# Optimization experiments

Measured on AMD Instinct MI355X. Metric: run time of the kernel, lower is better.

## Reference

```python
import jax, jax.numpy as jnp
import numpy as np

PC_RANGE = np.array([-15.0, -30.0, -2.0, 15.0, 30.0, 2.0], np.float32)
POST_CENTER = np.array([-20.0, -35.0, -20.0, -35.0, 20.0, 35.0, 20.0, 35.0], np.float32)
MAX_NUM = 100
NUM_CLASSES = 10
SCORE_THR = 0.1

_SX = PC_RANGE[3] - PC_RANGE[0]
_SY = PC_RANGE[4] - PC_RANGE[1]


def _denorm_bbox(b):
    # cxcywh -> xyxy, then scale x coords by pc_range x-extent, y by y-extent
    cx, cy, w, h = b[..., 0], b[..., 1], b[..., 2], b[..., 3]
    xyxy = jnp.stack([cx - w / 2, cy - h / 2, cx + w / 2, cy + h / 2], axis=-1)
    scale = jnp.asarray([_SX, _SY, _SX, _SY], jnp.float32)
    off = jnp.asarray([PC_RANGE[0], PC_RANGE[1], PC_RANGE[0], PC_RANGE[1]], jnp.float32)
    return xyxy * scale + off


def _denorm_pts(p):
    scale = jnp.asarray([_SX, _SY], jnp.float32)
    off = jnp.asarray([PC_RANGE[0], PC_RANGE[1]], jnp.float32)
    return p * scale + off


def _thresh_mask(scores):
    # torch: while thresh_mask.sum()==0: tmp*=0.9; if tmp<0.01: all-true; break
    s = jax.lax.stop_gradient(scores)
    mask0 = s > SCORE_THR

    def cond(state):
        _, m = state
        return jnp.sum(m) == 0

    def body(state):
        tmp, _ = state
        tmp = tmp * 0.9
        m = jnp.where(tmp < 0.01, s > -1.0, s >= tmp)
        return (tmp, m)

    _, mask = jax.lax.while_loop(cond, body, (jnp.asarray(SCORE_THR, jnp.float32), mask0))
    return mask


def _decode_single(cls, bbox, pts):
    # cls [Q,C], bbox [Q,4], pts [Q,P,2]
    flat = jax.nn.sigmoid(cls).reshape(-1)            # [Q*C]
    scores, idx = jax.lax.top_k(flat, MAX_NUM)        # [max_num]
    labels = idx % NUM_CLASSES
    bidx = idx // NUM_CLASSES
    boxes = _denorm_bbox(bbox[bidx])                  # [max_num,4]
    p = _denorm_pts(pts[bidx])                        # [max_num,P,2]
    tmask = _thresh_mask(scores)
    rmask = jnp.all(boxes >= POST_CENTER[:4], axis=-1) & jnp.all(boxes <= POST_CENTER[4:], axis=-1)
    mask = rmask & tmask
    # fixed-size output: zero-out entries the torch code would compact away,
    # and return the boolean keep-mask.
    return (
        jnp.where(mask[:, None], boxes, 0.0),
        jnp.where(mask, scores, 0.0),
        jnp.where(mask, labels, 0),
        jnp.where(mask[:, None, None], p, 0.0),
        mask,
    )


def setup_inputs() -> dict:
    key = jax.random.key(0)
    k1, k2, k3 = jax.random.split(key, 3)
    return {
        "cls_scores": jax.random.normal(k1, (8, 100000, 10), jnp.float32),
        "bbox_preds": jax.random.uniform(k2, (8, 100000, 4), jnp.float32),
        "pts_preds": jax.random.uniform(k3, (8, 100000, 20, 2), jnp.float32),
    }


def reference(cls_scores, bbox_preds, pts_preds):
    return jax.vmap(_decode_single)(cls_scores, bbox_preds, pts_preds)
```

## Files before the change

kernel.cpp:

```cpp
#include <hip/hip_runtime.h>
#include <stdint.h>

#define B 8
#define NQ 100000
#define NCLS 10
#define NELEM 1000000
#define NV4 250000
#define KTOP 100
#define NPTS 20
#define CAP 1024
#define THREADS 256
#define CBLOCKS 128
#define REG 64
#define T0 3.6f

__device__ __forceinline__ uint32_t fkey(float x) {
  uint32_t u = __float_as_uint(x);
  return (u & 0x80000000u) ? ~u : (u | 0x80000000u);
}

__device__ __forceinline__ uint64_t composite(float logit, uint32_t idx) {
  float s = 1.0f / (1.0f + expf(-logit));
  return ((uint64_t)__float_as_uint(s) << 32) | (uint64_t)(0xFFFFFFFFu - idx);
}

__global__ void collect_kernel(const float* __restrict__ cls,
                               uint32_t* __restrict__ counts,
                               uint64_t* __restrict__ cand) {
  __shared__ uint32_t lcnt;
  int b   = blockIdx.x / CBLOCKS;
  int sub = blockIdx.x % CBLOCKS;
  if (threadIdx.x == 0) lcnt = 0;
  __syncthreads();
  const float4* src = (const float4*)(cls + (size_t)b * NELEM);
  const int STRIDE = CBLOCKS * THREADS;
  int base = sub * THREADS + threadIdx.x;
  float4 v[8];
  int   idx[8];
#pragma unroll
  for (int k = 0; k < 8; ++k) {
    idx[k] = base + k * STRIDE;
    v[k] = (idx[k] < NV4) ? src[idx[k]] : make_float4(-100.f, -100.f, -100.f, -100.f);
  }
  uint64_t* region = cand + (size_t)(b * CBLOCKS + sub) * REG;
#pragma unroll
  for (int k = 0; k < 8; ++k) {
    float xs[4] = {v[k].x, v[k].y, v[k].z, v[k].w};
#pragma unroll
    for (int l = 0; l < 4; ++l) {
      if (xs[l] > T0) {
        uint32_t slot = atomicAdd(&lcnt, 1u);
        if (slot < REG)
          region[slot] = composite(xs[l], (uint32_t)(4 * idx[k] + l));
      }
    }
  }
  __syncthreads();
  if (threadIdx.x == 0) counts[b * CBLOCKS + sub] = lcnt;
}

__global__ void final_kernel(const float* __restrict__ cls,
                             const float* __restrict__ bbox,
                             const float* __restrict__ pts,
                             const uint32_t* __restrict__ counts,
                             const uint64_t* __restrict__ cand,
                             float* __restrict__ out) {
  __shared__ uint64_t s[CAP];
  __shared__ uint64_t s2[KTOP];
  __shared__ uint32_t sc[CBLOCKS];
  __shared__ uint32_t red[THREADS];
  __shared__ uint32_t s_bad, s_cnt;
  int b = blockIdx.x;
  int tid = threadIdx.x;

  if (tid == 0) s_bad = 0;
  __syncthreads();

  uint32_t myc = 0;
  if (tid < CBLOCKS) {
    myc = counts[b * CBLOCKS + tid];
    if (myc > REG) { s_bad = 1; myc = REG; }
    sc[tid] = myc;
  }
  for (int step = 1; step < CBLOCKS; step <<= 1) {
    __syncthreads();
    uint32_t add = (tid < CBLOCKS && tid >= step) ? sc[tid - step] : 0;
    __syncthreads();
    if (tid < CBLOCKS) sc[tid] += add;
  }
  __syncthreads();
  uint32_t total = sc[CBLOCKS - 1];
  uint32_t bad = s_bad || (total < KTOP) || (total > CAP);
  __syncthreads();

  uint32_t cnt;
  if (!bad) {
    if (tid < CBLOCKS) {
      uint32_t off = sc[tid] - myc;
      const uint64_t* region = cand + (size_t)(b * CBLOCKS + tid) * REG;
      for (uint32_t j = 0; j < myc; ++j) s[off + j] = region[j];
    }
    cnt = total;
  } else {
    const float* src = cls + (size_t)b * NELEM;
    uint32_t lo = 0, hi = 0xFFFFFFFFu;
    while (lo < hi) {
      uint32_t mid = lo + ((hi - lo + 1) >> 1);
      uint32_t c = 0;
      for (int i = tid; i < NELEM; i += THREADS)
        c += (fkey(src[i]) >= mid) ? 1u : 0u;
      red[tid] = c;
      __syncthreads();
      for (int off = THREADS / 2; off > 0; off >>= 1) {
        if (tid < off) red[tid] += red[tid + off];
        __syncthreads();
      }
      uint32_t totc = red[0];
      __syncthreads();
      if (totc >= KTOP) lo = mid; else hi = mid - 1;
    }
    uint32_t T = lo;
    if (tid == 0) s_cnt = 0;
    __syncthreads();
    for (int i = tid; i < NELEM; i += THREADS) {
      float x = src[i];
      if (fkey(x) > T) {
        uint32_t slot = atomicAdd(&s_cnt, 1u);
        s[slot] = composite(x, (uint32_t)i);
      }
    }
    __syncthreads();
    if (tid == 0) {
      uint32_t nGT = s_cnt, got = 0;
      for (int i = 0; i < NELEM && nGT + got < KTOP; ++i) {
        float x = src[i];
        if (fkey(x) == T) { s[nGT + got] = composite(x, (uint32_t)i); got++; }
      }
      s_cnt = KTOP;
    }
    __syncthreads();
    cnt = s_cnt;
  }
  __syncthreads();

  for (uint32_t i = tid; i < cnt; i += THREADS) {
    uint64_t me = s[i];
    uint32_t r = 0;
    for (uint32_t j = 0; j < cnt; ++j) r += (s[j] > me) ? 1u : 0u;
    if (r < KTOP) s2[r] = me;
  }
  __syncthreads();

  float smax = __uint_as_float((uint32_t)(s2[0] >> 32));
  int mode;
  float thr = 0.1f;
  if (smax > 0.1f) {
    mode = 0;
  } else {
    float tmp = 0.1f;
    mode = 2;
    while (true) {
      tmp *= 0.9f;
      if (tmp < 0.01f) { mode = 2; break; }
      if (smax >= tmp) { mode = 1; thr = tmp; break; }
    }
  }
  if (tid < KTOP) {
    uint64_t comp = s2[tid];
    float score = __uint_as_float((uint32_t)(comp >> 32));
    uint32_t idx = 0xFFFFFFFFu - (uint32_t)(comp & 0xFFFFFFFFu);
    uint32_t label = idx % NCLS;
    uint32_t bidx = idx / NCLS;
    if (bidx >= NQ) bidx = 0;
    float4 bb = ((const float4*)(bbox + (size_t)b * NQ * 4))[bidx];
    float hx = __fmul_rn(bb.z, 0.5f);
    float hy = __fmul_rn(bb.w, 0.5f);
    float x1 = __fadd_rn(__fmul_rn(__fsub_rn(bb.x, hx), 30.0f), -15.0f);
    float y1 = __fadd_rn(__fmul_rn(__fsub_rn(bb.y, hy), 60.0f), -30.0f);
    float x2 = __fadd_rn(__fmul_rn(__fadd_rn(bb.x, hx), 30.0f), -15.0f);
    float y2 = __fadd_rn(__fmul_rn(__fadd_rn(bb.y, hy), 60.0f), -30.0f);
    bool rmask = (x1 >= -20.0f) & (y1 >= -35.0f) & (x2 >= -20.0f) & (y2 >= -35.0f) &
                 (x1 <= 20.0f) & (y1 <= 35.0f) & (x2 <= 20.0f) & (y2 <= 35.0f);
    bool tmask = (mode == 2) || (mode == 0 ? (score > thr) : (score >= thr));
    bool mask = rmask && tmask;

    float* oBoxes  = out;
    float* oScores = out + B * KTOP * 4;
    float* oLabels = oScores + B * KTOP;
    float* oPts    = oLabels + B * KTOP;
    float* oMask   = oPts + B * KTOP * NPTS * 2;
    size_t rb = (size_t)b * KTOP + (size_t)tid;

    ((float4*)oBoxes)[rb] = mask ? make_float4(x1, y1, x2, y2)
                                 : make_float4(0.f, 0.f, 0.f, 0.f);
    oScores[rb] = mask ? score : 0.0f;
    oLabels[rb] = mask ? (float)label : 0.0f;
    oMask[rb]   = mask ? 1.0f : 0.0f;

    const float4* ps = (const float4*)(pts + (size_t)b * NQ * NPTS * 2 + (size_t)bidx * NPTS * 2);
    float4* po = (float4*)(oPts + rb * NPTS * 2);
#pragma unroll
    for (int j = 0; j < 10; ++j) {
      float4 p = ps[j];
      float4 o;
      o.x = __fadd_rn(__fmul_rn(p.x, 30.0f), -15.0f);
      o.y = __fadd_rn(__fmul_rn(p.y, 60.0f), -30.0f);
      o.z = __fadd_rn(__fmul_rn(p.z, 30.0f), -15.0f);
      o.w = __fadd_rn(__fmul_rn(p.w, 60.0f), -30.0f);
      po[j] = mask ? o : make_float4(0.f, 0.f, 0.f, 0.f);
    }
  }
}

extern "C" void kernel_launch(void* const* d_in, const int* in_sizes, int n_in,
                              void* d_out, int out_size, void* d_ws, size_t ws_size,
                              hipStream_t stream) {
  const float* cls  = (const float*)d_in[0];
  const float* bbox = (const float*)d_in[1];
  const float* pts  = (const float*)d_in[2];
  float* out = (float*)d_out;

  uint8_t* ws = (uint8_t*)d_ws;
  uint32_t* counts = (uint32_t*)ws;
  uint64_t* cand   = (uint64_t*)(ws + B * CBLOCKS * 4);

  collect_kernel<<<B * CBLOCKS, THREADS, 0, stream>>>(cls, counts, cand);
  final_kernel<<<B, THREADS, 0, stream>>>(cls, bbox, pts, counts, cand, out);
}
```

Measured before the change: 185.2 us.

## Restructure final kernel: wave-shuffle scan, prefetched candidates, gathers overlapped with rank sort

The final kernel's shared-memory Hillis-Steele prefix scan over per-block counts is replaced with a wavefront shuffle scan plus ballot, which removes many barriers. The first four candidates of each region are prefetched before the scan. Each thread now loads its candidate's bbox and point gathers before computing its rank, then scatters results by rank directly instead of going through a second sorted buffer. The candidate cap drops from 1024 to 256, so inputs with more candidates take the slow binary-search fallback more often, and p[10] held across the rank loop raises register use.

```diff
diff --git a/kernel.cpp b/kernel.cpp
--- a/kernel.cpp
+++ b/kernel.cpp
@@ -8,7 +8,7 @@
 #define NV4 250000
 #define KTOP 100
 #define NPTS 20
-#define CAP 1024
+#define CAP 256
 #define THREADS 256
 #define CBLOCKS 128
 #define REG 64
@@ -24,9 +24,10 @@
   return ((uint64_t)__float_as_uint(s) << 32) | (uint64_t)(0xFFFFFFFFu - idx);
 }
 
-__global__ void collect_kernel(const float* __restrict__ cls,
-                               uint32_t* __restrict__ counts,
-                               uint64_t* __restrict__ cand) {
+__global__ __launch_bounds__(THREADS)
+void collect_kernel(const float* __restrict__ cls,
+                    uint32_t* __restrict__ counts,
+                    uint64_t* __restrict__ cand) {
   __shared__ uint32_t lcnt;
   int b   = blockIdx.x / CBLOCKS;
   int sub = blockIdx.x % CBLOCKS;
@@ -59,60 +60,75 @@
   if (threadIdx.x == 0) counts[b * CBLOCKS + sub] = lcnt;
 }
 
-__global__ void final_kernel(const float* __restrict__ cls,
-                             const float* __restrict__ bbox,
-                             const float* __restrict__ pts,
-                             const uint32_t* __restrict__ counts,
-                             const uint64_t* __restrict__ cand,
-                             float* __restrict__ out) {
+__global__ __launch_bounds__(THREADS)
+void final_kernel(const float* __restrict__ cls,
+                  const float* __restrict__ bbox,
+                  const float* __restrict__ pts,
+                  const uint32_t* __restrict__ counts,
+                  const uint64_t* __restrict__ cand,
+                  float* __restrict__ out) {
   __shared__ uint64_t s[CAP];
-  __shared__ uint64_t s2[KTOP];
-  __shared__ uint32_t sc[CBLOCKS];
   __shared__ uint32_t red[THREADS];
-  __shared__ uint32_t s_bad, s_cnt;
-  int b = blockIdx.x;
-  int tid = threadIdx.x;
-
-  if (tid == 0) s_bad = 0;
-  __syncthreads();
-
-  uint32_t myc = 0;
+  __shared__ uint32_t s_wtot[2];
+  __shared__ uint32_t s_badw[2];
+  __shared__ uint32_t s_cnt;
+  __shared__ float    s_smax;
+  int b    = blockIdx.x;
+  int tid  = threadIdx.x;
+  int lane = tid & 63;
+  int wv   = tid >> 6;
+
+  uint32_t rawc = 0, myc = 0, npf = 0;
+  const uint64_t* region = nullptr;
+  uint64_t pf0 = 0, pf1 = 0, pf2 = 0, pf3 = 0;
   if (tid < CBLOCKS) {
-    myc = counts[b * CBLOCKS + tid];
-    if (myc > REG) { s_bad = 1; myc = REG; }
-    sc[tid] = myc;
-  }
-  for (int step = 1; step < CBLOCKS; step <<= 1) {
-    __syncthreads();
-    uint32_t add = (tid < CBLOCKS && tid >= step) ? sc[tid - step] : 0;
-    __syncthreads();
-    if (tid < CBLOCKS) sc[tid] += add;
-  }
-  __syncthreads();
-  uint32_t total = sc[CBLOCKS - 1];
-  uint32_t bad = s_bad || (total < KTOP) || (total > CAP);
-  __syncthreads();
+    rawc = counts[b * CBLOCKS + tid];
+    myc = rawc > REG ? REG : rawc;
+    region = cand + (size_t)(b * CBLOCKS + tid) * REG;
+    npf = myc < 4u ? myc : 4u;
+    if (npf > 0) pf0 = region[0];
+    if (npf > 1) pf1 = region[1];
+    if (npf > 2) pf2 = region[2];
+    if (npf > 3) pf3 = region[3];
+  }
+  uint32_t v = myc;
+#pragma unroll
+  for (int d = 1; d < 64; d <<= 1) {
+    uint32_t n = __shfl_up(v, d, 64);
+    if (lane >= d) v += n;
+  }
+  uint64_t wbad = __ballot(rawc > REG);
+  if (wv < 2) {
+    if (lane == 63) s_wtot[wv] = v;
+    if (lane == 0)  s_badw[wv] = (wbad != 0ull) ? 1u : 0u;
+  }
+  __syncthreads();
+  uint32_t total = s_wtot[0] + s_wtot[1];
+  bool bad = (s_badw[0] | s_badw[1]) || (total < KTOP) || (total > CAP);
 
   uint32_t cnt;
   if (!bad) {
     if (tid < CBLOCKS) {
-      uint32_t off = sc[tid] - myc;
-      const uint64_t* region = cand + (size_t)(b * CBLOCKS + tid) * REG;
-      for (uint32_t j = 0; j < myc; ++j) s[off + j] = region[j];
+      uint32_t off = (wv == 1 ? v + s_wtot[0] : v) - myc;
+      if (npf > 0) s[off + 0] = pf0;
+      if (npf > 1) s[off + 1] = pf1;
+      if (npf > 2) s[off + 2] = pf2;
+      if (npf > 3) s[off + 3] = pf3;
+      for (uint32_t j = npf; j < myc; ++j) s[off + j] = region[j];
     }
     cnt = total;
   } else {
     const float* src = cls + (size_t)b * NELEM;
     uint32_t lo = 0, hi = 0xFFFFFFFFu;
     while (lo < hi) {
-      uint32_t mid = lo + ((hi - lo + 1) >> 1);
+      uint32_t mid = (uint32_t)(((uint64_t)lo + (uint64_t)hi + 1ull) >> 1);
       uint32_t c = 0;
       for (int i = tid; i < NELEM; i += THREADS)
         c += (fkey(src[i]) >= mid) ? 1u : 0u;
       red[tid] = c;
       __syncthreads();
-      for (int off = THREADS / 2; off > 0; off >>= 1) {
-        if (tid < off) red[tid] += red[tid + off];
+      for (int off2 = THREADS / 2; off2 > 0; off2 >>= 1) {
+        if (tid < off2) red[tid] += red[tid + off2];
         __syncthreads();
       }
       uint32_t totc = red[0];
@@ -136,43 +152,48 @@
         float x = src[i];
         if (fkey(x) == T) { s[nGT + got] = composite(x, (uint32_t)i); got++; }
       }
-      s_cnt = KTOP;
-    }
-    __syncthreads();
-    cnt = s_cnt;
-  }
-  __syncthreads();
-
-  for (uint32_t i = tid; i < cnt; i += THREADS) {
-    uint64_t me = s[i];
-    uint32_t r = 0;
-    for (uint32_t j = 0; j < cnt; ++j) r += (s[j] > me) ? 1u : 0u;
-    if (r < KTOP) s2[r] = me;
-  }
-  __syncthreads();
-
-  float smax = __uint_as_float((uint32_t)(s2[0] >> 32));
-  int mode;
-  float thr = 0.1f;
-  if (smax > 0.1f) {
-    mode = 0;
-  } else {
-    float tmp = 0.1f;
-    mode = 2;
-    while (true) {
-      tmp *= 0.9f;
-      if (tmp < 0.01f) { mode = 2; break; }
-      if (smax >= tmp) { mode = 1; thr = tmp; break; }
-    }
-  }
-  if (tid < KTOP) {
-    uint64_t comp = s2[tid];
-    float score = __uint_as_float((uint32_t)(comp >> 32));
-    uint32_t idx = 0xFFFFFFFFu - (uint32_t)(comp & 0xFFFFFFFFu);
-    uint32_t label = idx % NCLS;
+    }
+    cnt = KTOP;
+  }
+  __syncthreads();
+
+  bool have = (tid < (int)cnt);
+  uint32_t r = 0, label = 0;
+  float score = 0.f;
+  float4 bb = make_float4(0.f, 0.f, 0.f, 0.f);
+  float4 p[10];
+  if (have) {
+    uint64_t me = s[tid];
+    score = __uint_as_float((uint32_t)(me >> 32));
+    uint32_t idx = 0xFFFFFFFFu - (uint32_t)(me & 0xFFFFFFFFu);
+    label = idx % NCLS;
     uint32_t bidx = idx / NCLS;
     if (bidx >= NQ) bidx = 0;
-    float4 bb = ((const float4*)(bbox + (size_t)b * NQ * 4))[bidx];
+    bb = ((const float4*)(bbox + (size_t)b * NQ * 4))[bidx];
+    const float4* ps = (const float4*)(pts + (size_t)b * NQ * NPTS * 2 +
+                                       (size_t)bidx * NPTS * 2);
+#pragma unroll
+    for (int j = 0; j < 10; ++j) p[j] = ps[j];
+    for (uint32_t j = 0; j < cnt; ++j) r += (s[j] > me) ? 1u : 0u;
+    if (r == 0) s_smax = score;
+  }
+  __syncthreads();
+
+  if (have && r < KTOP) {
+    float smax = s_smax;
+    int mode;
+    float thr = 0.1f;
+    if (smax > 0.1f) {
+      mode = 0;
+    } else {
+      float tmp = 0.1f;
+      mode = 2;
+      while (true) {
+        tmp *= 0.9f;
+        if (tmp < 0.01f) { mode = 2; break; }
+        if (smax >= tmp) { mode = 1; thr = tmp; break; }
+      }
+    }
     float hx = __fmul_rn(bb.z, 0.5f);
     float hy = __fmul_rn(bb.w, 0.5f);
     float x1 = __fadd_rn(__fmul_rn(__fsub_rn(bb.x, hx), 30.0f), -15.0f);
@@ -189,7 +210,7 @@
     float* oLabels = oScores + B * KTOP;
     float* oPts    = oLabels + B * KTOP;
     float* oMask   = oPts + B * KTOP * NPTS * 2;
-    size_t rb = (size_t)b * KTOP + (size_t)tid;
+    size_t rb = (size_t)b * KTOP + (size_t)r;
 
     ((float4*)oBoxes)[rb] = mask ? make_float4(x1, y1, x2, y2)
                                  : make_float4(0.f, 0.f, 0.f, 0.f);
@@ -197,16 +218,15 @@
     oLabels[rb] = mask ? (float)label : 0.0f;
     oMask[rb]   = mask ? 1.0f : 0.0f;
 
-    const float4* ps = (const float4*)(pts + (size_t)b * NQ * NPTS * 2 + (size_t)bidx * NPTS * 2);
     float4* po = (float4*)(oPts + rb * NPTS * 2);
 #pragma unroll
     for (int j = 0; j < 10; ++j) {
-      float4 p = ps[j];
+      float4 q = p[j];
       float4 o;
-      o.x = __fadd_rn(__fmul_rn(p.x, 30.0f), -15.0f);
-      o.y = __fadd_rn(__fmul_rn(p.y, 60.0f), -30.0f);
-      o.z = __fadd_rn(__fmul_rn(p.z, 30.0f), -15.0f);
-      o.w = __fadd_rn(__fmul_rn(p.w, 60.0f), -30.0f);
+      o.x = __fadd_rn(__fmul_rn(q.x, 30.0f), -15.0f);
+      o.y = __fadd_rn(__fmul_rn(q.y, 60.0f), -30.0f);
+      o.z = __fadd_rn(__fmul_rn(q.z, 30.0f), -15.0f);
+      o.w = __fadd_rn(__fmul_rn(q.w, 60.0f), -30.0f);
       po[j] = mask ? o : make_float4(0.f, 0.f, 0.f, 0.f);
     }
   }
```

After: 187.1 us. No clear change (+1.0%).
